# Kernel optimization log

Hardware: AMD Instinct MI355X
Metric: run time of the kernel (lower is better)

Reference implementation:

```python
import jax, jax.numpy as jnp
import numpy as np

B, C, H, W = 8, 256, 32, 32
N = H * W  # 1024; conv1 maps C -> N channels so all bmms are [B,N,N]


def setup_inputs() -> dict:
    key = jax.random.key(0)
    ks = jax.random.split(key, 11)
    s = 0.02  # weight scale to keep softmax logits in a sane range
    return {
        "x":     jax.random.normal(ks[0], (B, C, H, W), jnp.float32),
        "w1":    jax.random.normal(ks[1], (N, C), jnp.float32) * s,
        "b1":    jax.random.normal(ks[2], (N,), jnp.float32) * s,
        "wq":    jax.random.normal(ks[3], (N, N), jnp.float32) * s,
        "bq":    jax.random.normal(ks[4], (N,), jnp.float32) * s,
        "wv":    jax.random.normal(ks[5], (N, N), jnp.float32) * s,
        "bv":    jax.random.normal(ks[6], (N,), jnp.float32) * s,
        "w2":    jax.random.normal(ks[7], (C, N), jnp.float32) * s,
        "b2":    jax.random.normal(ks[8], (C,), jnp.float32) * s,
        "alpha": jax.random.normal(ks[9], (1,), jnp.float32),
        "beta":  jax.random.normal(ks[10], (1,), jnp.float32),
    }


def reference(x, w1, b1, wq, bq, wv, bv, w2, b2, alpha, beta):
    b, c, h, w = x.shape
    n = h * w
    # 1x1 convs as channel matmuls
    x1 = jnp.einsum('bchw,nc->bnhw', x, w1) + b1[None, :, None, None]  # [B,N,H,W]
    g = (jnp.einsum('bnhw,mn->bmhw', x1, wq) + bq[None, :, None, None]).reshape(b, n, n)
    r = (jnp.einsum('bnhw,mn->bmhw', x1, wv) + bv[None, :, None, None]).reshape(b, n, n)
    xf = x1.reshape(b, n, n)          # m^T in the torch code: [B, N_chan, HW]
    m = xf.transpose(0, 2, 1)         # m: [B, HW, N_chan]
    # spatial attention: z_s = softmax(m^T @ g)
    z_s = jax.nn.softmax(jnp.matmul(xf, g), axis=-1)            # [B,N,N]
    # channel attention: z_c = softmax(g^T @ m)
    z_c = jax.nn.softmax(jnp.matmul(g.transpose(0, 2, 1), m), axis=-1)  # [B,N,N]
    p_s = jnp.matmul(z_s, r)                                    # [B,N,HW]
    p_c = jnp.matmul(z_c, m).transpose(0, 2, 1)                 # [B,N,HW]
    p = (alpha[0] * p_s + beta[0] * p_c).reshape(b, n, h, w)
    out = jnp.einsum('bnhw,cn->bchw', p, w2) + b2[None, :, None, None]
    return out
```

## Files before the change

kernel.cpp:

```cpp
#include <hip/hip_runtime.h>
#include <hip/hip_bf16.h>


typedef __attribute__((ext_vector_type(4))) float f4;
typedef __attribute__((ext_vector_type(8))) short s8;
typedef __attribute__((ext_vector_type(4))) unsigned short us4;
typedef __attribute__((ext_vector_type(8))) unsigned short us8;

__device__ __forceinline__ unsigned short f2bf(float f) {
    __hip_bfloat16 h = __float2bfloat16(f);
    return __builtin_bit_cast(unsigned short, h);
}

#define GAS(p) ((const __attribute__((address_space(1))) unsigned int*)(p))
#define LAS(p) ((__attribute__((address_space(3))) unsigned int*)(p))

__global__ __launch_bounds__(256) void conv_weights(
    const float* __restrict__ w1, const float* __restrict__ wq,
    const float* __restrict__ wv, const float* __restrict__ w2,
    unsigned short* __restrict__ w1b, unsigned short* __restrict__ wqb,
    unsigned short* __restrict__ wvb, unsigned short* __restrict__ w2b,
    const float* __restrict__ bq, const float* __restrict__ bv,
    float* __restrict__ biasqv)
{
    long i = (long)blockIdx.x * 256 + threadIdx.x;
    if (i >= 655360) {
        long j = i - 655360;
        if (j < 512) {
            f4 v = (j < 256) ? ((const f4*)bq)[j] : ((const f4*)bv)[j - 256];
            ((f4*)biasqv)[j] = v;
        }
        return;
    }
    const float* src; unsigned short* dst; long base;
    if (i < 65536)               { src = w1; dst = w1b; base = 0; }
    else if (i < 65536+262144)   { src = wq; dst = wqb; base = 65536; }
    else if (i < 65536+524288)   { src = wv; dst = wvb; base = 65536+262144; }
    else                         { src = w2; dst = w2b; base = 65536+524288; }
    long j = i - base;
    f4 v = ((const f4*)src)[j];
    us4 o;
    #pragma unroll
    for (int k = 0; k < 4; ++k) o[k] = f2bf(v[k]);
    ((us4*)dst)[j] = o;
}

__global__ __launch_bounds__(256) void transpose_x(
    const float* __restrict__ x, unsigned short* __restrict__ xT)
{
    __shared__ float tl[32][33];
    const int b  = blockIdx.z;
    const int q0 = blockIdx.x * 32;
    const int c0 = blockIdx.y * 32;
    const int tx = threadIdx.x & 31, ty = threadIdx.x >> 5;
    #pragma unroll
    for (int j = 0; j < 4; ++j)
        tl[ty + j*8][tx] = x[((long)(b*256 + c0 + ty + j*8))*1024 + q0 + tx];
    __syncthreads();
    #pragma unroll
    for (int j = 0; j < 4; ++j)
        xT[((long)(b*1024 + q0 + ty + j*8))*256 + c0 + tx] = f2bf(tl[tx][ty + j*8]);
}

template<int BIAS, int OUTF32, int SPLIT, int NPASS>
__global__ __launch_bounds__(512, 2) void gemm256(
    const unsigned short* __restrict__ A0, const unsigned short* __restrict__ Bt0,
    const unsigned short* __restrict__ A1, const unsigned short* __restrict__ Bt1,
    long sA, long sB, int lda, int ldb,
    void* __restrict__ Cv0, void* __restrict__ Cv1, long sC, int ldc,
    const float* __restrict__ bias, int nt1)
{
    __shared__ __align__(16) unsigned short As[3][16384];
    __shared__ __align__(16) unsigned short Bs[3][8192];

    const int gx = gridDim.x, gy = gridDim.y;
    const int nwg = gx * gy * gridDim.z;
    int d = blockIdx.x + gx * (blockIdx.y + gy * blockIdx.z);
    int swz = (d & 7) * (nwg >> 3) + (d >> 3);
    const int bx = swz % gx; int tq = swz / gx;
    const int by = tq % gy;  const int bz = tq / gy;

    const int b  = bz;
    const int m0 = by * 256;
    const int n0 = bx * 128;
    const int t  = threadIdx.x;
    const int w  = t >> 6, l = t & 63;
    const int wr = w >> 1, wc = w & 1;
    const int lr = l & 15, lg = l >> 4;

    const unsigned short* A0b = A0  + (long)b * sA;
    const unsigned short* B0b = Bt0 + (long)b * sB;
    const unsigned short* A1b = (NPASS > 1) ? A1  + (long)b * sA : nullptr;
    const unsigned short* B1b = (NPASS > 1) ? Bt1 + (long)b * sB : nullptr;

    const int rl  = l >> 3;
    const int gsw = ((l & 7) ^ (rl & 7)) * 8;

    const int NT = NPASS * nt1;

    auto stageA = [&](int sp, int bf) {
        const unsigned short* Ap = A0b; int kt = sp * 64;
        if (NPASS > 1 && sp >= nt1) { Ap = A1b; kt = (sp - nt1) * 64; }
        #pragma unroll
        for (int i = 0; i < 4; ++i) {
            const int rb = w*32 + i*8;
            __builtin_amdgcn_global_load_lds(GAS(Ap + (long)(m0 + rb + rl)*lda + kt + gsw),
                                             LAS(&As[bf][rb*64]), 16, 0, 0);
        }
    };
    auto stageB = [&](int sp, int bf) {
        const unsigned short* Bp = B0b; int kt = sp * 64;
        if (NPASS > 1 && sp >= nt1) { Bp = B1b; kt = (sp - nt1) * 64; }
        #pragma unroll
        for (int i = 0; i < 2; ++i) {
            const int rb = w*16 + i*8;
            __builtin_amdgcn_global_load_lds(GAS(Bp + (long)(n0 + rb + rl)*ldb + kt + gsw),
                                             LAS(&Bs[bf][rb*64]), 16, 0, 0);
        }
    };

    f4 acc[4][4];
    #pragma unroll
    for (int i = 0; i < 4; ++i)
        #pragma unroll
        for (int j = 0; j < 4; ++j) acc[i][j] = (f4){0.f, 0.f, 0.f, 0.f};

    stageA(0, 0); stageB(0, 0);
    stageA(1, 1); stageB(1, 1);

    int buf = 0;
    for (int s = 0; s < NT; ++s) {
        if (s + 1 < NT) asm volatile("s_waitcnt vmcnt(6)" ::: "memory");
        else            asm volatile("s_waitcnt vmcnt(0)" ::: "memory");
        __builtin_amdgcn_s_barrier();

        int bn = buf + 2; if (bn >= 3) bn -= 3;
        s8 aF[4], bF[4];

        #pragma unroll
        for (int m = 0; m < 4; ++m) {
            const int row = wr*64 + m*16 + lr;
            aF[m] = *(const s8*)&As[buf][row*64 + ((lg ^ (row & 7)) * 8)];
        }
        #pragma unroll
        for (int n = 0; n < 4; ++n) {
            const int row = wc*64 + n*16 + lr;
            bF[n] = *(const s8*)&Bs[buf][row*64 + ((lg ^ (row & 7)) * 8)];
        }
        if (s + 2 < NT) stageA(s + 2, bn);
        asm volatile("s_waitcnt lgkmcnt(0)" ::: "memory");
        __builtin_amdgcn_sched_barrier(0);
        __builtin_amdgcn_s_setprio(1);
        #pragma unroll
        for (int m = 0; m < 4; ++m)
            #pragma unroll
            for (int n = 0; n < 4; ++n)
                acc[m][n] = __builtin_amdgcn_mfma_f32_16x16x32_bf16(aF[m], bF[n], acc[m][n], 0, 0, 0);
        __builtin_amdgcn_s_setprio(0);

        #pragma unroll
        for (int m = 0; m < 4; ++m) {
            const int row = wr*64 + m*16 + lr;
            aF[m] = *(const s8*)&As[buf][row*64 + (((4 + lg) ^ (row & 7)) * 8)];
        }
        #pragma unroll
        for (int n = 0; n < 4; ++n) {
            const int row = wc*64 + n*16 + lr;
            bF[n] = *(const s8*)&Bs[buf][row*64 + (((4 + lg) ^ (row & 7)) * 8)];
        }
        if (s + 2 < NT) stageB(s + 2, bn);
        asm volatile("s_waitcnt lgkmcnt(0)" ::: "memory");
        __builtin_amdgcn_sched_barrier(0);
        __builtin_amdgcn_s_setprio(1);
        #pragma unroll
        for (int m = 0; m < 4; ++m)
            #pragma unroll
            for (int n = 0; n < 4; ++n)
                acc[m][n] = __builtin_amdgcn_mfma_f32_16x16x32_bf16(aF[m], bF[n], acc[m][n], 0, 0, 0);
        __builtin_amdgcn_s_setprio(0);

        if (++buf == 3) buf = 0;
    }

    void* Cd = Cv0; int nbase = n0;
    if (SPLIT && n0 >= 1024) { Cd = Cv1; nbase = n0 - 1024; }

    const int rbase = lg * 4;
    #pragma unroll
    for (int m = 0; m < 4; ++m) {
        #pragma unroll
        for (int n = 0; n < 4; ++n) {
            const int row  = m0 + wr*64 + m*16 + rbase;
            const int col  = nbase + wc*64 + n*16 + lr;
            const int bcol = n0    + wc*64 + n*16 + lr;
            #pragma unroll
            for (int j = 0; j < 4; ++j) {
                float v = acc[m][n][j];
                if (BIAS == 1) v += bias[row + j];
                else if (BIAS == 2) v += bias[bcol];
                const long idx = (long)b*sC + (long)(row + j)*ldc + col;
                if (OUTF32) ((float*)Cd)[idx] = v;
                else ((unsigned short*)Cd)[idx] = f2bf(v);
            }
        }
    }
}

template<int BIAS, int OUTF32, int NT1, int NBUF>
__global__ __launch_bounds__(256) void gemm_pipe(
    const unsigned short* __restrict__ A0, const unsigned short* __restrict__ Bt0,
    long sA, long sB, int lda, int ldb,
    void* __restrict__ Cv0, long sC, int ldc,
    const float* __restrict__ bias)
{
    constexpr int NT = NT1;
    __shared__ __align__(16) unsigned short As[NBUF][4096];
    __shared__ __align__(16) unsigned short Bs[NBUF][4096];

    const int gx = gridDim.x, gy = gridDim.y;
    const int nwg = gx * gy * gridDim.z;
    int d = blockIdx.x + gx * (blockIdx.y + gy * blockIdx.z);
    int swz = (d & 7) * (nwg >> 3) + (d >> 3);
    const int bx = swz % gx; int tq = swz / gx;
    const int by = tq % gy;  const int bz = tq / gy;

    const int b  = bz;
    const int m0 = by * 128;
    const int n0 = bx * 128;
    const int t  = threadIdx.x;
    const int w  = t >> 6, l = t & 63;
    const int wr = w >> 1, wc = w & 1;
    const int lr = l & 15;

    const unsigned short* A0b = A0  + (long)b * sA;
    const unsigned short* B0b = Bt0 + (long)b * sB;

    const int rA   = w*32 + (l >> 2);
    const int cswz = ((l & 3) ^ ((l >> 3) & 3)) * 8;
    const int swzr = (((l >> 4) ^ ((lr >> 1) & 3)) * 8);

    f4 acc[4][4];
    #pragma unroll
    for (int i = 0; i < 4; ++i)
        #pragma unroll
        for (int j = 0; j < 4; ++j) acc[i][j] = (f4){0.f, 0.f, 0.f, 0.f};

    auto stage = [&](int sp, int bf) {
        const int kt = sp * 32;
        __builtin_amdgcn_global_load_lds(GAS(A0b + (long)(m0 + rA     )*lda + kt + cswz), LAS(&As[bf][w*1024      ]), 16, 0, 0);
        __builtin_amdgcn_global_load_lds(GAS(A0b + (long)(m0 + rA + 16)*lda + kt + cswz), LAS(&As[bf][w*1024 + 512]), 16, 0, 0);
        __builtin_amdgcn_global_load_lds(GAS(B0b + (long)(n0 + rA     )*ldb + kt + cswz), LAS(&Bs[bf][w*1024      ]), 16, 0, 0);
        __builtin_amdgcn_global_load_lds(GAS(B0b + (long)(n0 + rA + 16)*ldb + kt + cswz), LAS(&Bs[bf][w*1024 + 512]), 16, 0, 0);
    };

    #pragma unroll
    for (int dpl = 0; dpl < NBUF - 1; ++dpl) stage(dpl, dpl);

    int buf = 0;
    for (int s = 0; s < NT; ++s) {
        if (NBUF >= 4 && s + 2 < NT) asm volatile("s_waitcnt vmcnt(8)" ::: "memory");
        else if (s + 1 < NT)         asm volatile("s_waitcnt vmcnt(4)" ::: "memory");
        else                         asm volatile("s_waitcnt vmcnt(0)" ::: "memory");
        __builtin_amdgcn_s_barrier();
        __builtin_amdgcn_sched_barrier(0);

        s8 aF[4], bF[4];
        #pragma unroll
        for (int m = 0; m < 4; ++m) aF[m] = *(const s8*)&As[buf][(wr*64 + m*16 + lr)*32 + swzr];
        #pragma unroll
        for (int n = 0; n < 4; ++n) bF[n] = *(const s8*)&Bs[buf][(wc*64 + n*16 + lr)*32 + swzr];

        if (s + NBUF - 1 < NT) {
            int bn = buf + NBUF - 1; if (bn >= NBUF) bn -= NBUF;
            stage(s + NBUF - 1, bn);
        }

        __builtin_amdgcn_s_setprio(1);
        #pragma unroll
        for (int m = 0; m < 4; ++m)
            #pragma unroll
            for (int n = 0; n < 4; ++n)
                acc[m][n] = __builtin_amdgcn_mfma_f32_16x16x32_bf16(aF[m], bF[n], acc[m][n], 0, 0, 0);
        __builtin_amdgcn_s_setprio(0);

        if (++buf == NBUF) buf = 0;
    }

    const int rbase = (l >> 4) * 4;
    #pragma unroll
    for (int m = 0; m < 4; ++m) {
        #pragma unroll
        for (int n = 0; n < 4; ++n) {
            const int row = m0 + wr*64 + m*16 + rbase;
            const int col = n0 + wc*64 + n*16 + lr;
            #pragma unroll
            for (int j = 0; j < 4; ++j) {
                float v = acc[m][n][j];
                if (BIAS == 1) v += bias[row + j];
                else if (BIAS == 2) v += bias[col];
                const long idx = (long)b*sC + (long)(row + j)*ldc + col;
                if (OUTF32) ((float*)Cv0)[idx] = v;
                else ((unsigned short*)Cv0)[idx] = f2bf(v);
            }
        }
    }
}

__global__ __launch_bounds__(256) void row_softmax(
    const float* __restrict__ S, unsigned short* __restrict__ Z,
    const float* __restrict__ scale_p)
{
    const int wid = threadIdx.x >> 6, l = threadIdx.x & 63;
    const long row = (long)blockIdx.x * 4 + wid;
    const float* src = S + row * 1024;
    f4 v[4];
    #pragma unroll
    for (int i = 0; i < 4; ++i) v[i] = *(const f4*)&src[(i*64 + l)*4];
    float m = -3.4e38f;
    #pragma unroll
    for (int i = 0; i < 4; ++i)
        #pragma unroll
        for (int j = 0; j < 4; ++j) m = fmaxf(m, v[i][j]);
    #pragma unroll
    for (int off = 32; off; off >>= 1) m = fmaxf(m, __shfl_xor(m, off));
    float s = 0.f;
    #pragma unroll
    for (int i = 0; i < 4; ++i)
        #pragma unroll
        for (int j = 0; j < 4; ++j) { v[i][j] = __expf(v[i][j] - m); s += v[i][j]; }
    #pragma unroll
    for (int off = 32; off; off >>= 1) s += __shfl_xor(s, off);
    const float c = scale_p[0] / s;
    #pragma unroll
    for (int i = 0; i < 4; ++i) {
        us4 o;
        #pragma unroll
        for (int j = 0; j < 4; ++j) o[j] = f2bf(v[i][j] * c);
        *(us4*)&Z[row*1024 + (long)(i*64 + l)*4] = o;
    }
}

__global__ __launch_bounds__(256) void col_stats(
    const float* __restrict__ S, float* __restrict__ cm, float* __restrict__ cs)
{
    __shared__ float pm[4][64], ps[4][64];
    const int b  = blockIdx.y;
    const int ci = threadIdx.x & 63, ks = threadIdx.x >> 6;
    const int q  = blockIdx.x * 64 + ci;
    const float* Sb = S + (long)b * 1048576 + q;
    float m = -3.4e38f, s = 0.f;
    for (int k = ks*256; k < ks*256 + 256; ++k) {
        float v = Sb[(long)k * 1024];
        float dlt = v - m;
        float ed = __expf(-fabsf(dlt));
        if (dlt > 0.f) { s = s * ed + 1.f; m = v; } else s += ed;
    }
    pm[ks][ci] = m; ps[ks][ci] = s;
    __syncthreads();
    if (threadIdx.x < 64) {
        float M = pm[0][ci];
        #pragma unroll
        for (int i = 1; i < 4; ++i) M = fmaxf(M, pm[i][ci]);
        float Ssum = 0.f;
        #pragma unroll
        for (int i = 0; i < 4; ++i) Ssum += ps[i][ci] * __expf(pm[i][ci] - M);
        cm[b*1024 + q] = M;
        cs[b*1024 + q] = Ssum;
    }
}

__global__ __launch_bounds__(256) void col_write(
    const float* __restrict__ S, const float* __restrict__ cm,
    const float* __restrict__ cs, unsigned short* __restrict__ Z,
    const float* __restrict__ scale_p)
{
    const int b  = blockIdx.z;
    const int k0 = blockIdx.y * 64;
    const int q  = blockIdx.x * 256 + threadIdx.x;
    const float m   = cm[b*1024 + q];
    const float inv = scale_p[0] / cs[b*1024 + q];
    const float* Sb = S + (long)b * 1048576 + q;
    unsigned short* Zb = Z + (long)b * 1048576 + (long)q * 1024 + k0;
    #pragma unroll
    for (int c8 = 0; c8 < 8; ++c8) {
        us8 o;
        #pragma unroll
        for (int j = 0; j < 8; ++j)
            o[j] = f2bf(inv * __expf(Sb[(long)(k0 + c8*8 + j) * 1024] - m));
        *(us8*)&Zb[c8*8] = o;
    }
}

extern "C" void kernel_launch(void* const* d_in, const int* in_sizes, int n_in,
                              void* d_out, int out_size, void* d_ws, size_t ws_size,
                              hipStream_t stream)
{
    const float* x     = (const float*)d_in[0];
    const float* w1    = (const float*)d_in[1];
    const float* b1    = (const float*)d_in[2];
    const float* wq    = (const float*)d_in[3];
    const float* bq    = (const float*)d_in[4];
    const float* wv    = (const float*)d_in[5];
    const float* bv    = (const float*)d_in[6];
    const float* w2    = (const float*)d_in[7];
    const float* b2    = (const float*)d_in[8];
    const float* alpha = (const float*)d_in[9];
    const float* beta  = (const float*)d_in[10];
    float* out = (float*)d_out;

    char* ws = (char*)d_ws;
    size_t off = 0;
    auto alloc = [&](size_t bytes) -> void* {
        void* p = ws + off; off += (bytes + 255) & ~(size_t)255; return p;
    };
    unsigned short* w1b   = (unsigned short*)alloc(1024L*256*2);
    unsigned short* wqvb  = (unsigned short*)alloc(2048L*1024*2);
    unsigned short* w2b   = (unsigned short*)alloc(256L*1024*2);
    float*          biasqv= (float*)alloc(2048L*4);
    float*          cmv   = (float*)alloc(8L*1024*4);
    float*          csv   = (float*)alloc(8L*1024*4);
    unsigned short* xTb   = (unsigned short*)alloc(8L*1024*256*2);
    unsigned short* x1b   = (unsigned short*)alloc(8L*1024*1024*2);
    unsigned short* x1tb  = (unsigned short*)alloc(8L*1024*1024*2);
    unsigned short* gtb   = (unsigned short*)alloc(8L*1024*1024*2);
    unsigned short* rtb   = (unsigned short*)alloc(8L*1024*1024*2);
    float*          Sf    = (float*)alloc(8L*1024*1024*4);
    unsigned short* zsb = x1tb;
    unsigned short* zcb = gtb;
    unsigned short* Ptb = (unsigned short*)Sf;

    const long S1M = 1048576;

    conv_weights<<<2562, 256, 0, stream>>>(w1, wq, wv, w2, w1b, wqvb, wqvb + S1M, w2b, bq, bv, biasqv);
    transpose_x<<<dim3(32, 8, 8), 256, 0, stream>>>(x, xTb);

    gemm256<1,0,0,1><<<dim3(8, 4, 8), 512, 0, stream>>>(
        w1b, xTb, nullptr, nullptr, 0, 262144, 256, 256, x1b, nullptr, S1M, 1024, b1, 4);
    gemm256<2,0,0,1><<<dim3(8, 32, 1), 512, 0, stream>>>(
        xTb, w1b, nullptr, nullptr, 0, 0, 256, 256, x1tb, nullptr, 0, 1024, b1, 4);
    gemm256<2,0,1,1><<<dim3(16, 32, 1), 512, 0, stream>>>(
        x1tb, wqvb, nullptr, nullptr, 0, 0, 1024, 1024, gtb, rtb, 0, 1024, biasqv, 16);
    gemm256<0,1,0,1><<<dim3(8, 4, 8), 512, 0, stream>>>(
        x1b, gtb, nullptr, nullptr, S1M, S1M, 1024, 1024, Sf, nullptr, S1M, 1024, nullptr, 16);
    row_softmax<<<2048, 256, 0, stream>>>(Sf, zsb, alpha);
    col_stats<<<dim3(16, 8), 256, 0, stream>>>(Sf, cmv, csv);
    col_write<<<dim3(4, 16, 8), 256, 0, stream>>>(Sf, cmv, csv, zcb, beta);
    gemm256<0,0,0,2><<<dim3(8, 4, 8), 512, 0, stream>>>(
        rtb, zsb, zcb, x1b, S1M, S1M, 1024, 1024, Ptb, nullptr, S1M, 1024, nullptr, 16);
    gemm_pipe<1,1,32,4><<<dim3(8, 2, 8), 256, 0, stream>>>(
        w2b, Ptb, 0, S1M, 1024, 1024, out, 262144, 1024, b2);
}
```

Baseline: 189.0 us.

## Restructure 256x128 GEMM to four waves with larger per-wave tiles and BK=32

```diff
diff --git a/kernel.cpp b/kernel.cpp
--- a/kernel.cpp
+++ b/kernel.cpp
@@ -63,15 +63,15 @@
 }
 
 template<int BIAS, int OUTF32, int SPLIT, int NPASS>
-__global__ __launch_bounds__(512, 2) void gemm256(
+__global__ __launch_bounds__(256, 2) void gemm_w4(
     const unsigned short* __restrict__ A0, const unsigned short* __restrict__ Bt0,
     const unsigned short* __restrict__ A1, const unsigned short* __restrict__ Bt1,
     long sA, long sB, int lda, int ldb,
     void* __restrict__ Cv0, void* __restrict__ Cv1, long sC, int ldc,
     const float* __restrict__ bias, int nt1)
 {
-    __shared__ __align__(16) unsigned short As[3][16384];
-    __shared__ __align__(16) unsigned short Bs[3][8192];
+    __shared__ __align__(16) unsigned short As[3][8192];
+    __shared__ __align__(16) unsigned short Bs[3][4096];
 
     const int gx = gridDim.x, gy = gridDim.y;
     const int nwg = gx * gy * gridDim.z;
@@ -93,92 +93,69 @@
     const unsigned short* A1b = (NPASS > 1) ? A1  + (long)b * sA : nullptr;
     const unsigned short* B1b = (NPASS > 1) ? Bt1 + (long)b * sB : nullptr;
 
-    const int rl  = l >> 3;
-    const int gsw = ((l & 7) ^ (rl & 7)) * 8;
+    const int rl4 = l >> 2;
+    const int gsw = ((l & 3) ^ (rl4 & 3)) * 8;
 
     const int NT = NPASS * nt1;
 
-    auto stageA = [&](int sp, int bf) {
-        const unsigned short* Ap = A0b; int kt = sp * 64;
-        if (NPASS > 1 && sp >= nt1) { Ap = A1b; kt = (sp - nt1) * 64; }
+    auto stage = [&](int sp, int bf) {
+        const unsigned short* Ap = A0b; const unsigned short* Bp = B0b;
+        int kt = sp * 32;
+        if (NPASS > 1 && sp >= nt1) { Ap = A1b; Bp = B1b; kt = (sp - nt1) * 32; }
         #pragma unroll
         for (int i = 0; i < 4; ++i) {
-            const int rb = w*32 + i*8;
-            __builtin_amdgcn_global_load_lds(GAS(Ap + (long)(m0 + rb + rl)*lda + kt + gsw),
-                                             LAS(&As[bf][rb*64]), 16, 0, 0);
+            const int rb = w*64 + i*16;
+            __builtin_amdgcn_global_load_lds(GAS(Ap + (long)(m0 + rb + rl4)*lda + kt + gsw),
+                                             LAS(&As[bf][rb*32]), 16, 0, 0);
+        }
+        #pragma unroll
+        for (int i = 0; i < 2; ++i) {
+            const int rb = w*32 + i*16;
+            __builtin_amdgcn_global_load_lds(GAS(Bp + (long)(n0 + rb + rl4)*ldb + kt + gsw),
+                                             LAS(&Bs[bf][rb*32]), 16, 0, 0);
         }
     };
-    auto stageB = [&](int sp, int bf) {
-        const unsigned short* Bp = B0b; int kt = sp * 64;
-        if (NPASS > 1 && sp >= nt1) { Bp = B1b; kt = (sp - nt1) * 64; }
-        #pragma unroll
-        for (int i = 0; i < 2; ++i) {
-            const int rb = w*16 + i*8;
-            __builtin_amdgcn_global_load_lds(GAS(Bp + (long)(n0 + rb + rl)*ldb + kt + gsw),
-                                             LAS(&Bs[bf][rb*64]), 16, 0, 0);
-        }
-    };
-
-    f4 acc[4][4];
-    #pragma unroll
-    for (int i = 0; i < 4; ++i)
+
+    f4 acc[8][4];
+    #pragma unroll
+    for (int i = 0; i < 8; ++i)
         #pragma unroll
         for (int j = 0; j < 4; ++j) acc[i][j] = (f4){0.f, 0.f, 0.f, 0.f};
 
-    stageA(0, 0); stageB(0, 0);
-    stageA(1, 1); stageB(1, 1);
+    stage(0, 0);
+    stage(1, 1);
+
+    const int swzc = ((lg ^ (lr & 3)) * 8);
 
     int buf = 0;
     for (int s = 0; s < NT; ++s) {
         if (s + 1 < NT) asm volatile("s_waitcnt vmcnt(6)" ::: "memory");
         else            asm volatile("s_waitcnt vmcnt(0)" ::: "memory");
         __builtin_amdgcn_s_barrier();
-
-        int bn = buf + 2; if (bn >= 3) bn -= 3;
-        s8 aF[4], bF[4];
-
-        #pragma unroll
-        for (int m = 0; m < 4; ++m) {
-            const int row = wr*64 + m*16 + lr;
-            aF[m] = *(const s8*)&As[buf][row*64 + ((lg ^ (row & 7)) * 8)];
+        __builtin_amdgcn_sched_barrier(0);
+
+        s8 aF[8], bF[4];
+        #pragma unroll
+        for (int m = 0; m < 8; ++m) {
+            const int R = wr*128 + m*16 + lr;
+            aF[m] = *(const s8*)&As[buf][R*32 + swzc];
         }
         #pragma unroll
         for (int n = 0; n < 4; ++n) {
-            const int row = wc*64 + n*16 + lr;
-            bF[n] = *(const s8*)&Bs[buf][row*64 + ((lg ^ (row & 7)) * 8)];
-        }
-        if (s + 2 < NT) stageA(s + 2, bn);
-        asm volatile("s_waitcnt lgkmcnt(0)" ::: "memory");
-        __builtin_amdgcn_sched_barrier(0);
+            const int R = wc*64 + n*16 + lr;
+            bF[n] = *(const s8*)&Bs[buf][R*32 + swzc];
+        }
+
+        if (s + 2 < NT) { int bn = buf + 2; if (bn >= 3) bn -= 3; stage(s + 2, bn); }
+
         __builtin_amdgcn_s_setprio(1);
         #pragma unroll
-        for (int m = 0; m < 4; ++m)
+        for (int m = 0; m < 8; ++m)
             #pragma unroll
             for (int n = 0; n < 4; ++n)
                 acc[m][n] = __builtin_amdgcn_mfma_f32_16x16x32_bf16(aF[m], bF[n], acc[m][n], 0, 0, 0);
         __builtin_amdgcn_s_setprio(0);
 
-        #pragma unroll
-        for (int m = 0; m < 4; ++m) {
-            const int row = wr*64 + m*16 + lr;
-            aF[m] = *(const s8*)&As[buf][row*64 + (((4 + lg) ^ (row & 7)) * 8)];
-        }
-        #pragma unroll
-        for (int n = 0; n < 4; ++n) {
-            const int row = wc*64 + n*16 + lr;
-            bF[n] = *(const s8*)&Bs[buf][row*64 + (((4 + lg) ^ (row & 7)) * 8)];
-        }
-        if (s + 2 < NT) stageB(s + 2, bn);
-        asm volatile("s_waitcnt lgkmcnt(0)" ::: "memory");
-        __builtin_amdgcn_sched_barrier(0);
-        __builtin_amdgcn_s_setprio(1);
-        #pragma unroll
-        for (int m = 0; m < 4; ++m)
-            #pragma unroll
-            for (int n = 0; n < 4; ++n)
-                acc[m][n] = __builtin_amdgcn_mfma_f32_16x16x32_bf16(aF[m], bF[n], acc[m][n], 0, 0, 0);
-        __builtin_amdgcn_s_setprio(0);
-
         if (++buf == 3) buf = 0;
     }
 
@@ -187,10 +164,10 @@
 
     const int rbase = lg * 4;
     #pragma unroll
-    for (int m = 0; m < 4; ++m) {
+    for (int m = 0; m < 8; ++m) {
         #pragma unroll
         for (int n = 0; n < 4; ++n) {
-            const int row  = m0 + wr*64 + m*16 + rbase;
+            const int row  = m0 + wr*128 + m*16 + rbase;
             const int col  = nbase + wc*64 + n*16 + lr;
             const int bcol = n0    + wc*64 + n*16 + lr;
             #pragma unroll
@@ -434,19 +411,19 @@
     conv_weights<<<2562, 256, 0, stream>>>(w1, wq, wv, w2, w1b, wqvb, wqvb + S1M, w2b, bq, bv, biasqv);
     transpose_x<<<dim3(32, 8, 8), 256, 0, stream>>>(x, xTb);
 
-    gemm256<1,0,0,1><<<dim3(8, 4, 8), 512, 0, stream>>>(
-        w1b, xTb, nullptr, nullptr, 0, 262144, 256, 256, x1b, nullptr, S1M, 1024, b1, 4);
-    gemm256<2,0,0,1><<<dim3(8, 32, 1), 512, 0, stream>>>(
-        xTb, w1b, nullptr, nullptr, 0, 0, 256, 256, x1tb, nullptr, 0, 1024, b1, 4);
-    gemm256<2,0,1,1><<<dim3(16, 32, 1), 512, 0, stream>>>(
-        x1tb, wqvb, nullptr, nullptr, 0, 0, 1024, 1024, gtb, rtb, 0, 1024, biasqv, 16);
-    gemm256<0,1,0,1><<<dim3(8, 4, 8), 512, 0, stream>>>(
-        x1b, gtb, nullptr, nullptr, S1M, S1M, 1024, 1024, Sf, nullptr, S1M, 1024, nullptr, 16);
+    gemm_w4<1,0,0,1><<<dim3(8, 4, 8), 256, 0, stream>>>(
+        w1b, xTb, nullptr, nullptr, 0, 262144, 256, 256, x1b, nullptr, S1M, 1024, b1, 8);
+    gemm_w4<2,0,0,1><<<dim3(8, 32, 1), 256, 0, stream>>>(
+        xTb, w1b, nullptr, nullptr, 0, 0, 256, 256, x1tb, nullptr, 0, 1024, b1, 8);
+    gemm_w4<2,0,1,1><<<dim3(16, 32, 1), 256, 0, stream>>>(
+        x1tb, wqvb, nullptr, nullptr, 0, 0, 1024, 1024, gtb, rtb, 0, 1024, biasqv, 32);
+    gemm_w4<0,1,0,1><<<dim3(8, 4, 8), 256, 0, stream>>>(
+        x1b, gtb, nullptr, nullptr, S1M, S1M, 1024, 1024, Sf, nullptr, S1M, 1024, nullptr, 32);
     row_softmax<<<2048, 256, 0, stream>>>(Sf, zsb, alpha);
     col_stats<<<dim3(16, 8), 256, 0, stream>>>(Sf, cmv, csv);
     col_write<<<dim3(4, 16, 8), 256, 0, stream>>>(Sf, cmv, csv, zcb, beta);
-    gemm256<0,0,0,2><<<dim3(8, 4, 8), 512, 0, stream>>>(
-        rtb, zsb, zcb, x1b, S1M, S1M, 1024, 1024, Ptb, nullptr, S1M, 1024, nullptr, 16);
+    gemm_w4<0,0,0,2><<<dim3(8, 4, 8), 256, 0, stream>>>(
+        rtb, zsb, zcb, x1b, S1M, S1M, 1024, 1024, Ptb, nullptr, S1M, 1024, nullptr, 32);
     gemm_pipe<1,1,32,4><<<dim3(8, 2, 8), 256, 0, stream>>>(
         w2b, Ptb, 0, S1M, 1024, 1024, out, 262144, 1024, b2);
 }
```

New measurement: 208.5 us. 10.3% more time.

## Software-pipeline LDS fragment reads with MFMA via register double-buffering in GEMM loop

Applied to the files above, without the earlier changes.

```diff
diff --git a/kernel.cpp b/kernel.cpp
--- a/kernel.cpp
+++ b/kernel.cpp
@@ -127,59 +127,87 @@
 
     stageA(0, 0); stageB(0, 0);
     stageA(1, 1); stageB(1, 1);
+    asm volatile("s_waitcnt vmcnt(6)" ::: "memory");
+    __builtin_amdgcn_sched_barrier(0);
+    __builtin_amdgcn_s_barrier();
+
+    s8 a0[4], b0[4], a1f[4], b1f[4];
+
+    #pragma unroll
+    for (int m = 0; m < 4; ++m) {
+        const int R = wr*64 + m*16 + lr;
+        a0[m] = *(const s8*)&As[0][R*64 + ((lg ^ (R & 7)) * 8)];
+    }
+    #pragma unroll
+    for (int n = 0; n < 4; ++n) {
+        const int R = wc*64 + n*16 + lr;
+        b0[n] = *(const s8*)&Bs[0][R*64 + ((lg ^ (R & 7)) * 8)];
+    }
+    asm volatile("s_waitcnt lgkmcnt(0)" ::: "memory");
+    __builtin_amdgcn_sched_barrier(0);
 
     int buf = 0;
     for (int s = 0; s < NT; ++s) {
-        if (s + 1 < NT) asm volatile("s_waitcnt vmcnt(6)" ::: "memory");
-        else            asm volatile("s_waitcnt vmcnt(0)" ::: "memory");
-        __builtin_amdgcn_s_barrier();
-
         int bn = buf + 2; if (bn >= 3) bn -= 3;
-        s8 aF[4], bF[4];
+        int bx1 = buf + 1; if (bx1 >= 3) bx1 -= 3;
 
         #pragma unroll
         for (int m = 0; m < 4; ++m) {
-            const int row = wr*64 + m*16 + lr;
-            aF[m] = *(const s8*)&As[buf][row*64 + ((lg ^ (row & 7)) * 8)];
+            const int R = wr*64 + m*16 + lr;
+            a1f[m] = *(const s8*)&As[buf][R*64 + (((4 + lg) ^ (R & 7)) * 8)];
         }
         #pragma unroll
         for (int n = 0; n < 4; ++n) {
-            const int row = wc*64 + n*16 + lr;
-            bF[n] = *(const s8*)&Bs[buf][row*64 + ((lg ^ (row & 7)) * 8)];
+            const int R = wc*64 + n*16 + lr;
+            b1f[n] = *(const s8*)&Bs[buf][R*64 + (((4 + lg) ^ (R & 7)) * 8)];
         }
         if (s + 2 < NT) stageA(s + 2, bn);
+        __builtin_amdgcn_s_setprio(1);
+        #pragma unroll
+        for (int m = 0; m < 4; ++m)
+            #pragma unroll
+            for (int n = 0; n < 4; ++n)
+                acc[m][n] = __builtin_amdgcn_mfma_f32_16x16x32_bf16(a0[m], b0[n], acc[m][n], 0, 0, 0);
+        __builtin_amdgcn_s_setprio(0);
         asm volatile("s_waitcnt lgkmcnt(0)" ::: "memory");
         __builtin_amdgcn_sched_barrier(0);
-        __builtin_amdgcn_s_setprio(1);
-        #pragma unroll
-        for (int m = 0; m < 4; ++m)
-            #pragma unroll
-            for (int n = 0; n < 4; ++n)
-                acc[m][n] = __builtin_amdgcn_mfma_f32_16x16x32_bf16(aF[m], bF[n], acc[m][n], 0, 0, 0);
-        __builtin_amdgcn_s_setprio(0);
-
-        #pragma unroll
-        for (int m = 0; m < 4; ++m) {
-            const int row = wr*64 + m*16 + lr;
-            aF[m] = *(const s8*)&As[buf][row*64 + (((4 + lg) ^ (row & 7)) * 8)];
-        }
-        #pragma unroll
-        for (int n = 0; n < 4; ++n) {
-            const int row = wc*64 + n*16 + lr;
-            bF[n] = *(const s8*)&Bs[buf][row*64 + (((4 + lg) ^ (row & 7)) * 8)];
-        }
-        if (s + 2 < NT) stageB(s + 2, bn);
-        asm volatile("s_waitcnt lgkmcnt(0)" ::: "memory");
-        __builtin_amdgcn_sched_barrier(0);
-        __builtin_amdgcn_s_setprio(1);
-        #pragma unroll
-        for (int m = 0; m < 4; ++m)
-            #pragma unroll
-            for (int n = 0; n < 4; ++n)
-                acc[m][n] = __builtin_amdgcn_mfma_f32_16x16x32_bf16(aF[m], bF[n], acc[m][n], 0, 0, 0);
-        __builtin_amdgcn_s_setprio(0);
-
-        if (++buf == 3) buf = 0;
+
+        if (s + 1 < NT) {
+            if (s + 2 < NT) asm volatile("s_waitcnt vmcnt(4)" ::: "memory");
+            else            asm volatile("s_waitcnt vmcnt(0)" ::: "memory");
+            __builtin_amdgcn_sched_barrier(0);
+            __builtin_amdgcn_s_barrier();
+            #pragma unroll
+            for (int m = 0; m < 4; ++m) {
+                const int R = wr*64 + m*16 + lr;
+                a0[m] = *(const s8*)&As[bx1][R*64 + ((lg ^ (R & 7)) * 8)];
+            }
+            #pragma unroll
+            for (int n = 0; n < 4; ++n) {
+                const int R = wc*64 + n*16 + lr;
+                b0[n] = *(const s8*)&Bs[bx1][R*64 + ((lg ^ (R & 7)) * 8)];
+            }
+            if (s + 2 < NT) stageB(s + 2, bn);
+            __builtin_amdgcn_s_setprio(1);
+            #pragma unroll
+            for (int m = 0; m < 4; ++m)
+                #pragma unroll
+                for (int n = 0; n < 4; ++n)
+                    acc[m][n] = __builtin_amdgcn_mfma_f32_16x16x32_bf16(a1f[m], b1f[n], acc[m][n], 0, 0, 0);
+            __builtin_amdgcn_s_setprio(0);
+            asm volatile("s_waitcnt lgkmcnt(0)" ::: "memory");
+            __builtin_amdgcn_sched_barrier(0);
+        } else {
+            __builtin_amdgcn_s_setprio(1);
+            #pragma unroll
+            for (int m = 0; m < 4; ++m)
+                #pragma unroll
+                for (int n = 0; n < 4; ++n)
+                    acc[m][n] = __builtin_amdgcn_mfma_f32_16x16x32_bf16(a1f[m], b1f[n], acc[m][n], 0, 0, 0);
+            __builtin_amdgcn_s_setprio(0);
+        }
+
+        buf = bx1;
     }
 
     void* Cd = Cv0; int nbase = n0;
```

After: 188.2 us. No clear change (-0.4%).
